# Kernel optimization log

Measured on AMD Instinct MI355X. Metric: run time of the kernel, lower is better.

Reference implementation:

```python
import jax, jax.numpy as jnp
from jax import lax
import numpy as np

LAM = 0.95          # config.agent.return_lambda
HORIZON = 333.0     # config.agent.horizon
# slowtar=True, contdisc=False

B, T, D, H = 1024, 16, 5120, 1024


def _mlp(feat, w1, b1, w2, b2, w3, b3):
    # critic MLP -> scalar mean per (b, t); [B,T,D] -> [B,T]
    h = jax.nn.silu(jnp.einsum('btd,dh->bth', feat, w1) + b1)
    h = jax.nn.silu(jnp.einsum('bth,hk->btk', h, w2) + b2)
    return jnp.einsum('bth,h->bt', h, w3) + b3[0]


def setup_inputs() -> dict:
    key = jax.random.key(0)
    ks = jax.random.split(key, 10)
    sc1 = 1.0 / np.sqrt(D)
    sc2 = 1.0 / np.sqrt(H)
    return {
        'feat': jax.random.normal(ks[0], (B, T, D), jnp.float32),
        'rew': jax.random.normal(ks[1], (B, T), jnp.float32),
        'cont': jax.random.uniform(ks[2], (B, T), jnp.float32),
        'net_w1': jax.random.normal(ks[3], (D, H), jnp.float32) * sc1,
        'net_b1': jnp.zeros((H,), jnp.float32),
        'net_w2': jax.random.normal(ks[4], (H, H), jnp.float32) * sc2,
        'net_b2': jnp.zeros((H,), jnp.float32),
        'net_w3': jax.random.normal(ks[5], (H,), jnp.float32) * sc2,
        'net_b3': jnp.zeros((1,), jnp.float32),
        'slow_w1': jax.random.normal(ks[6], (D, H), jnp.float32) * sc1,
        'slow_b1': jnp.zeros((H,), jnp.float32),
        'slow_w2': jax.random.normal(ks[7], (H, H), jnp.float32) * sc2,
        'slow_b2': jnp.zeros((H,), jnp.float32),
        'slow_w3': jax.random.normal(ks[8], (H,), jnp.float32) * sc2,
        'slow_b3': jnp.zeros((1,), jnp.float32),
        'voffset': jax.random.normal(ks[9], (1,), jnp.float32),
        'vscale': jax.random.uniform(jax.random.fold_in(key, 99), (1,), jnp.float32, minval=0.5, maxval=1.5),
    }


def reference(feat, rew, cont, net_w1, net_b1, net_w2, net_b2, net_w3, net_b3,
              slow_w1, slow_b1, slow_w2, slow_b2, slow_w3, slow_b3, voffset, vscale):
    critic = _mlp(feat, net_w1, net_b1, net_w2, net_b2, net_w3, net_b3)        # [B,T]
    slowcritic = _mlp(feat, slow_w1, slow_b1, slow_w2, slow_b2, slow_w3, slow_b3)
    val = critic * vscale[0] + voffset[0]
    slowval = slowcritic * vscale[0] + voffset[0]
    tarval = slowval  # slowtar = True
    discount = 1.0 - 1.0 / HORIZON  # contdisc = False
    disc = cont[:, 1:] * discount                                 # [B,T-1]
    interm = rew[:, 1:] + (1.0 - LAM) * disc * tarval[:, 1:]      # [B,T-1]

    def step(carry, xs):
        i_t, d_t = xs
        r = i_t + d_t * LAM * carry
        return r, r

    # reversed linear recurrence over time: rets[t] = interm[t] + disc[t]*lam*rets[t+1]
    _, ys = lax.scan(step, tarval[:, -1], (interm.T, disc.T), reverse=True)  # [T-1,B]
    ret = ys.T                                                    # [B,T-1]
    return rew, ret, tarval, critic, slowcritic
```

## Files before the change

### kernel.cpp

```cpp
#include <hip/hip_runtime.h>
#include <stdint.h>

typedef unsigned short u16;
typedef __attribute__((ext_vector_type(8))) __bf16 bf16x8;
typedef __attribute__((ext_vector_type(8))) u16 u16x8;
typedef __attribute__((ext_vector_type(4))) u16 u16x4;
typedef __attribute__((ext_vector_type(4))) float f32x4;

#define LAM 0.95f
#define DISCOUNT (1.0f - 1.0f / 333.0f)

constexpr int Bsz = 1024, Tsz = 16, Dsz = 5120, Hsz = 1024;
constexpr int Msz = Bsz * Tsz;
constexpr int Nsz = 2 * Hsz;
constexpr int ES = 136;

__device__ __forceinline__ u16 f2bf(float x) {
  union { float f; uint32_t u; } un; un.f = x;
  uint32_t u = un.u;
  return (u16)((u + 0x7FFFu + ((u >> 16) & 1u)) >> 16);
}
__device__ __forceinline__ void async16(const void* g, void* l) {
  __builtin_amdgcn_global_load_lds(
      (const __attribute__((address_space(1))) uint32_t*)g,
      (__attribute__((address_space(3))) uint32_t*)l, 16, 0, 0);
}

__global__ __launch_bounds__(256) void transpose_cvt(
    const float* __restrict__ src, u16* __restrict__ dst, int K, int N) {
  __shared__ float tile[64][65];
  int k0 = blockIdx.x * 64, n0 = blockIdx.y * 64;
  int tid = threadIdx.x;
#pragma unroll
  for (int i = 0; i < 4; ++i) {
    int idx = i * 256 + tid, rr = idx >> 4, c4 = (idx & 15) * 4;
    float4 v = *(const float4*)&src[(size_t)(k0 + rr) * N + n0 + c4];
    tile[rr][c4 + 0] = v.x; tile[rr][c4 + 1] = v.y;
    tile[rr][c4 + 2] = v.z; tile[rr][c4 + 3] = v.w;
  }
  __syncthreads();
#pragma unroll
  for (int i = 0; i < 4; ++i) {
    int idx = i * 256 + tid, rr = idx >> 4, c4 = (idx & 15) * 4;
    u16x4 o;
    o[0] = f2bf(tile[c4 + 0][rr]); o[1] = f2bf(tile[c4 + 1][rr]);
    o[2] = f2bf(tile[c4 + 2][rr]); o[3] = f2bf(tile[c4 + 3][rr]);
    *(u16x4*)&dst[(size_t)(n0 + rr) * K + k0 + c4] = o;
  }
}

__global__ void prep_small(const float* nb1, const float* sb1, const float* nb2,
                           const float* sb2, const float* nw3, const float* sw3,
                           float* bias1, float* bias2, float* w3cat,
                           float* accN, float* accS) {
  int i = blockIdx.x * 256 + threadIdx.x;
  if (i < 1024) { bias1[i] = nb1[i]; bias2[i] = nb2[i]; w3cat[i] = nw3[i]; }
  else if (i < 2048) { bias1[i] = sb1[i - 1024]; bias2[i] = sb2[i - 1024]; w3cat[i] = sw3[i - 1024]; }
  for (int j = i; j < Msz; j += gridDim.x * 256) { accN[j] = 0.f; accS[j] = 0.f; }
}

__global__ void cvt_f32_to_bf16(const float* __restrict__ src, u16* __restrict__ dst, int n4) {
  int i = blockIdx.x * 256 + threadIdx.x;
  int stride = gridDim.x * 256;
  for (; i < n4; i += stride) {
    float4 v = ((const float4*)src)[i];
    u16x4 o; o[0] = f2bf(v.x); o[1] = f2bf(v.y); o[2] = f2bf(v.z); o[3] = f2bf(v.w);
    ((u16x4*)dst)[i] = o;
  }
}

template <int MODE, bool A_F32>
__global__ __launch_bounds__(256) void gemm_fused(
    const void* __restrict__ Ap, const u16* __restrict__ Bp,
    const float* __restrict__ bias, u16* __restrict__ Out,
    const float* __restrict__ w3cat, float* __restrict__ accN, float* __restrict__ accS,
    int K, int lda, int a_half_off) {
  __shared__ __align__(16) u16 smem[(MODE == 0) ? (128 * ES) : 16384];
  u16* ldsA = smem;
  u16* ldsB = smem + 8192;

  const int tid = threadIdx.x;
  const int lane = tid & 63;
  const int wv = tid >> 6;
  const int wm = (wv >> 1) << 6;
  const int wn = (wv & 1) << 6;
  const int lm = lane & 15, lq = lane >> 4, l7 = lane & 7;

  const int blk = blockIdx.x;
  const int xcd = blk & 7;
  const int l = blk >> 3;
  const int quad = l >> 6;
  const int mi = l & 7, ni = (l >> 3) & 7;
  const int mt = xcd * 16 + ((quad & 1) << 3) + mi;
  const int nt = ((quad >> 1) << 3) + ni;
  const int m0 = mt << 7, n0 = nt << 7;
  const int a_off = (n0 >= Hsz) ? a_half_off : 0;

  const u16* bsrc[4];
  const float* asrcf[4];
  const u16* asrcb[4];
  u16* ldsAd[4];
  u16* ldsBd[4];
#pragma unroll
  for (int i = 0; i < 4; ++i) {
    int cid = i * 256 + tid;
    int row = cid >> 3, ch = cid & 7;
    int kp = ch ^ (row & 7);
    bsrc[i] = Bp + (size_t)(n0 + row) * K + kp * 8;
    if (A_F32) asrcf[i] = (const float*)Ap + (size_t)(m0 + row) * lda + a_off + kp * 8;
    else       asrcb[i] = (const u16*)Ap + (size_t)(m0 + row) * lda + a_off + kp * 8;
    ldsAd[i] = &ldsA[cid * 8];
    ldsBd[i] = &ldsB[cid * 8];
  }

  int rA[4], rB[4];
#pragma unroll
  for (int t = 0; t < 4; ++t) {
    rA[t] = (wm + t * 16 + lm) * 64;
    rB[t] = (wn + t * 16 + lm) * 64;
  }

  f32x4 acc[4][4];
#pragma unroll
  for (int a = 0; a < 4; ++a)
#pragma unroll
    for (int b = 0; b < 4; ++b) acc[a][b] = f32x4{0.f, 0.f, 0.f, 0.f};

  for (int kt = 0; kt < K; kt += 64) {
#pragma unroll
    for (int i = 0; i < 4; ++i) async16(bsrc[i] + kt, ldsBd[i]);
    if (A_F32) {
      float4 v0[4], v1[4];
#pragma unroll
      for (int i = 0; i < 4; ++i) {
        const float* p = asrcf[i] + kt;
        v0[i] = *(const float4*)p;
        v1[i] = *(const float4*)(p + 4);
      }
#pragma unroll
      for (int i = 0; i < 4; ++i) {
        u16x8 pk;
        pk[0] = f2bf(v0[i].x); pk[1] = f2bf(v0[i].y); pk[2] = f2bf(v0[i].z); pk[3] = f2bf(v0[i].w);
        pk[4] = f2bf(v1[i].x); pk[5] = f2bf(v1[i].y); pk[6] = f2bf(v1[i].z); pk[7] = f2bf(v1[i].w);
        *(u16x8*)ldsAd[i] = pk;
      }
    } else {
#pragma unroll
      for (int i = 0; i < 4; ++i) async16(asrcb[i] + kt, ldsAd[i]);
    }
    __syncthreads();
#pragma unroll
    for (int ks = 0; ks < 2; ++ks) {
      const int ck = ((ks << 2) + lq) ^ l7;
      bf16x8 af[4], bfr[4];
#pragma unroll
      for (int t = 0; t < 4; ++t) af[t] = *(const bf16x8*)&ldsA[rA[t] + ck * 8];
#pragma unroll
      for (int t = 0; t < 4; ++t) bfr[t] = *(const bf16x8*)&ldsB[rB[t] + ck * 8];
#pragma unroll
      for (int a = 0; a < 4; ++a)
#pragma unroll
        for (int b = 0; b < 4; ++b)
          acc[a][b] = __builtin_amdgcn_mfma_f32_16x16x32_bf16(bfr[b], af[a], acc[a][b], 0, 0, 0);
    }
    __syncthreads();
  }

  if (MODE == 0) {
#pragma unroll
    for (int a = 0; a < 4; ++a) {
      int ml = wm + a * 16 + lm;
#pragma unroll
      for (int b = 0; b < 4; ++b) {
        int nb = wn + b * 16 + lq * 4;
        u16x4 pk;
#pragma unroll
        for (int rr = 0; rr < 4; ++rr) {
          float v = acc[a][b][rr] + bias[n0 + nb + rr];
          v = v * (1.0f / (1.0f + __expf(-v)));
          pk[rr] = f2bf(v);
        }
        *(u16x4*)&smem[ml * ES + nb] = pk;
      }
    }
    __syncthreads();
#pragma unroll
    for (int i = 0; i < 8; ++i) {
      int r = i * 16 + (tid >> 4);
      int c = (tid & 15) * 8;
      u16x8 vv = *(const u16x8*)&smem[r * ES + c];
      *(u16x8*)&Out[(size_t)(m0 + r) * Nsz + n0 + c] = vv;
    }
  } else {
    float pr[4] = {0.f, 0.f, 0.f, 0.f};
#pragma unroll
    for (int a = 0; a < 4; ++a) {
#pragma unroll
      for (int b = 0; b < 4; ++b) {
        int nb = n0 + wn + b * 16 + lq * 4;
#pragma unroll
        for (int rr = 0; rr < 4; ++rr) {
          float v = acc[a][b][rr] + bias[nb + rr];
          v = v * (1.0f / (1.0f + __expf(-v)));
          pr[a] += v * w3cat[nb + rr];
        }
      }
    }
    float* accp = (n0 < Hsz) ? accN : accS;
#pragma unroll
    for (int a = 0; a < 4; ++a) {
      pr[a] += __shfl_xor(pr[a], 16);
      pr[a] += __shfl_xor(pr[a], 32);
      if (lq == 0) atomicAdd(&accp[m0 + wm + a * 16 + lm], pr[a]);
    }
  }
}

__global__ void finalize_scan(const float* __restrict__ accN, const float* __restrict__ accS,
                              const float* __restrict__ nb3, const float* __restrict__ sb3,
                              const float* __restrict__ voff, const float* __restrict__ vscl,
                              const float* __restrict__ rew, const float* __restrict__ cont,
                              float* __restrict__ o_rew, float* __restrict__ o_ret,
                              float* __restrict__ o_tar, float* __restrict__ o_cri,
                              float* __restrict__ o_slo) {
  __shared__ float star[Tsz], srew[Tsz], scont[Tsz];
  int b = blockIdx.x;
  int t = threadIdx.x;
  if (t < Tsz) {
    int m = b * Tsz + t;
    float c = accN[m] + nb3[0];
    float s = accS[m] + sb3[0];
    float tv = s * vscl[0] + voff[0];
    o_cri[m] = c; o_slo[m] = s; o_tar[m] = tv;
    float rw = rew[m];
    o_rew[m] = rw;
    star[t] = tv; srew[t] = rw; scont[t] = cont[m];
  }
  __syncthreads();
  if (t == 0) {
    float carry = star[Tsz - 1];
    for (int k = Tsz - 2; k >= 0; --k) {
      float d = scont[k + 1] * DISCOUNT;
      carry = srew[k + 1] + (1.0f - LAM) * d * star[k + 1] + d * LAM * carry;
      o_ret[b * (Tsz - 1) + k] = carry;
    }
  }
}

constexpr size_t WT1_OFF = 0;
constexpr size_t WT1_BYTES = (size_t)Nsz * Dsz * 2;
constexpr size_t WT2_OFF = WT1_OFF + WT1_BYTES;
constexpr size_t WT2_BYTES = (size_t)Nsz * Hsz * 2;
constexpr size_t B1_OFF = WT2_OFF + WT2_BYTES;
constexpr size_t B2_OFF = B1_OFF + 8192;
constexpr size_t W3_OFF = B2_OFF + 8192;
constexpr size_t ACCN_OFF = W3_OFF + 8192;
constexpr size_t ACCS_OFF = ACCN_OFF + (size_t)Msz * 4;
constexpr size_t H1_OFF = ACCS_OFF + (size_t)Msz * 4;
constexpr size_t H_BYTES = (size_t)Msz * Nsz * 2;
constexpr size_t FEATB_OFF = H1_OFF + H_BYTES;
constexpr size_t FEATB_BYTES = (size_t)Msz * Dsz * 2;
constexpr size_t NEED_BIG = FEATB_OFF + FEATB_BYTES;

extern "C" void kernel_launch(void* const* d_in, const int* in_sizes, int n_in,
                              void* d_out, int out_size, void* d_ws, size_t ws_size,
                              hipStream_t stream) {
  const float* feat = (const float*)d_in[0];
  const float* rew  = (const float*)d_in[1];
  const float* cont = (const float*)d_in[2];
  const float* nw1  = (const float*)d_in[3];
  const float* nb1  = (const float*)d_in[4];
  const float* nw2  = (const float*)d_in[5];
  const float* nb2  = (const float*)d_in[6];
  const float* nw3  = (const float*)d_in[7];
  const float* nb3  = (const float*)d_in[8];
  const float* sw1  = (const float*)d_in[9];
  const float* sb1  = (const float*)d_in[10];
  const float* sw2  = (const float*)d_in[11];
  const float* sb2  = (const float*)d_in[12];
  const float* sw3  = (const float*)d_in[13];
  const float* sb3  = (const float*)d_in[14];
  const float* voff = (const float*)d_in[15];
  const float* vscl = (const float*)d_in[16];

  char* ws = (char*)d_ws;
  u16* wt1 = (u16*)(ws + WT1_OFF);
  u16* wt2 = (u16*)(ws + WT2_OFF);
  float* bias1 = (float*)(ws + B1_OFF);
  float* bias2 = (float*)(ws + B2_OFF);
  float* w3cat = (float*)(ws + W3_OFF);
  float* accN = (float*)(ws + ACCN_OFF);
  float* accS = (float*)(ws + ACCS_OFF);
  u16* h1 = (u16*)(ws + H1_OFF);
  u16* featb = (u16*)(ws + FEATB_OFF);
  const bool big = ws_size >= NEED_BIG;

  float* out = (float*)d_out;
  float* o_rew = out;
  float* o_ret = out + 16384;
  float* o_tar = out + 31744;
  float* o_cri = out + 48128;
  float* o_slo = out + 64512;

  transpose_cvt<<<dim3(Dsz / 64, Hsz / 64), 256, 0, stream>>>(nw1, wt1, Dsz, Hsz);
  transpose_cvt<<<dim3(Dsz / 64, Hsz / 64), 256, 0, stream>>>(sw1, wt1 + (size_t)Hsz * Dsz, Dsz, Hsz);
  transpose_cvt<<<dim3(Hsz / 64, Hsz / 64), 256, 0, stream>>>(nw2, wt2, Hsz, Hsz);
  transpose_cvt<<<dim3(Hsz / 64, Hsz / 64), 256, 0, stream>>>(sw2, wt2 + (size_t)Hsz * Hsz, Hsz, Hsz);
  prep_small<<<8, 256, 0, stream>>>(nb1, sb1, nb2, sb2, nw3, sw3, bias1, bias2, w3cat, accN, accS);

  const int gemm_grid = (Msz / 128) * (Nsz / 128);
  if (big) {
    cvt_f32_to_bf16<<<4096, 256, 0, stream>>>(feat, featb, Msz * Dsz / 4);
    gemm_fused<0, false><<<gemm_grid, 256, 0, stream>>>(
        featb, wt1, bias1, h1, nullptr, nullptr, nullptr, Dsz, Dsz, 0);
  } else {
    gemm_fused<0, true><<<gemm_grid, 256, 0, stream>>>(
        feat, wt1, bias1, h1, nullptr, nullptr, nullptr, Dsz, Dsz, 0);
  }
  gemm_fused<1, false><<<gemm_grid, 256, 0, stream>>>(
      h1, wt2, bias2, nullptr, w3cat, accN, accS, Hsz, Nsz, Hsz);
  finalize_scan<<<Bsz, 64, 0, stream>>>(accN, accS, nb3, sb3, voff, vscl, rew, cont,
                                        o_rew, o_ret, o_tar, o_cri, o_slo);
}
```

Before: 1.043 ms.

## Add dedicated 256x128-tile GEMM1 kernel with XCD-aware block mapping

New measurement: 1.268 ms. +21.5%, slower.

```diff
diff --git a/kernel.cpp b/kernel.cpp
--- a/kernel.cpp
+++ b/kernel.cpp
@@ -66,6 +66,119 @@
     float4 v = ((const float4*)src)[i];
     u16x4 o; o[0] = f2bf(v.x); o[1] = f2bf(v.y); o[2] = f2bf(v.z); o[3] = f2bf(v.w);
     ((u16x4*)dst)[i] = o;
+  }
+}
+
+__global__ __launch_bounds__(256) void gemm1_k(
+    const u16* __restrict__ Ap, const u16* __restrict__ Bp,
+    const float* __restrict__ bias, u16* __restrict__ Out, int K) {
+  __shared__ __align__(16) u16 smem[24576];
+  u16* ldsA = smem;
+  u16* ldsB = smem + 16384;
+
+  const int tid = threadIdx.x;
+  const int lane = tid & 63;
+  const int wv = tid >> 6;
+  const int wm = (wv >> 1) * 128;
+  const int wn = (wv & 1) * 64;
+  const int lm = lane & 15, lq = lane >> 4, l7 = lane & 7;
+
+  const int blk = blockIdx.x;
+  const int xcd = blk & 7;
+  const int l = blk >> 3;
+  const int half_ = l >> 6;
+  const int mi = l & 7, ni = (l >> 3) & 7;
+  const int m0 = (xcd * 8 + mi) << 8;
+  const int n0 = ((half_ << 3) + ni) << 7;
+
+  const u16* asrc[8]; u16* ldsAd[8];
+  const u16* bsrc[4]; u16* ldsBd[4];
+#pragma unroll
+  for (int i = 0; i < 8; ++i) {
+    int cid = i * 256 + tid;
+    int row = cid >> 3, ch = cid & 7;
+    int kp = ch ^ (row & 7);
+    asrc[i] = Ap + (size_t)(m0 + row) * K + kp * 8;
+    ldsAd[i] = &ldsA[cid * 8];
+  }
+#pragma unroll
+  for (int i = 0; i < 4; ++i) {
+    int cid = i * 256 + tid;
+    int row = cid >> 3, ch = cid & 7;
+    int kp = ch ^ (row & 7);
+    bsrc[i] = Bp + (size_t)(n0 + row) * K + kp * 8;
+    ldsBd[i] = &ldsB[cid * 8];
+  }
+
+  int rA[8], rB[4];
+#pragma unroll
+  for (int t = 0; t < 8; ++t) rA[t] = (wm + t * 16 + lm) * 64;
+#pragma unroll
+  for (int t = 0; t < 4; ++t) rB[t] = (wn + t * 16 + lm) * 64;
+
+  f32x4 acc[8][4];
+#pragma unroll
+  for (int a = 0; a < 8; ++a)
+#pragma unroll
+    for (int b = 0; b < 4; ++b) acc[a][b] = f32x4{0.f, 0.f, 0.f, 0.f};
+
+  for (int kt = 0; kt < K; kt += 64) {
+#pragma unroll
+    for (int i = 0; i < 4; ++i) async16(bsrc[i] + kt, ldsBd[i]);
+#pragma unroll
+    for (int i = 0; i < 8; ++i) async16(asrc[i] + kt, ldsAd[i]);
+    __syncthreads();
+#pragma unroll
+    for (int ks = 0; ks < 2; ++ks) {
+      const int ck = ((ks << 2) + lq) ^ l7;
+      bf16x8 bfr[4];
+#pragma unroll
+      for (int t = 0; t < 4; ++t) bfr[t] = *(const bf16x8*)&ldsB[rB[t] + ck * 8];
+#pragma unroll
+      for (int h = 0; h < 2; ++h) {
+        bf16x8 af[4];
+#pragma unroll
+        for (int t = 0; t < 4; ++t) af[t] = *(const bf16x8*)&ldsA[rA[h * 4 + t] + ck * 8];
+#pragma unroll
+        for (int a = 0; a < 4; ++a)
+#pragma unroll
+          for (int b = 0; b < 4; ++b)
+            acc[h * 4 + a][b] =
+                __builtin_amdgcn_mfma_f32_16x16x32_bf16(bfr[b], af[a], acc[h * 4 + a][b], 0, 0, 0);
+      }
+    }
+    __syncthreads();
+  }
+
+#pragma unroll
+  for (int p = 0; p < 2; ++p) {
+    if ((wv >> 1) == p) {
+#pragma unroll
+      for (int a = 0; a < 8; ++a) {
+        int ml = a * 16 + lm;
+#pragma unroll
+        for (int b = 0; b < 4; ++b) {
+          int nb = wn + b * 16 + lq * 4;
+          u16x4 pk;
+#pragma unroll
+          for (int rr = 0; rr < 4; ++rr) {
+            float v = acc[a][b][rr] + bias[n0 + nb + rr];
+            v = v * (1.0f / (1.0f + __expf(-v)));
+            pk[rr] = f2bf(v);
+          }
+          *(u16x4*)&smem[ml * ES + nb] = pk;
+        }
+      }
+    }
+    __syncthreads();
+#pragma unroll
+    for (int i = 0; i < 8; ++i) {
+      int r = i * 16 + (tid >> 4);
+      int c = (tid & 15) * 8;
+      u16x8 vv = *(const u16x8*)&smem[r * ES + c];
+      *(u16x8*)&Out[(size_t)(m0 + p * 128 + r) * Nsz + n0 + c] = vv;
+    }
+    __syncthreads();
   }
 }
 
@@ -308,16 +421,14 @@
   transpose_cvt<<<dim3(Hsz / 64, Hsz / 64), 256, 0, stream>>>(sw2, wt2 + (size_t)Hsz * Hsz, Hsz, Hsz);
   prep_small<<<8, 256, 0, stream>>>(nb1, sb1, nb2, sb2, nw3, sw3, bias1, bias2, w3cat, accN, accS);
 
-  const int gemm_grid = (Msz / 128) * (Nsz / 128);
   if (big) {
     cvt_f32_to_bf16<<<4096, 256, 0, stream>>>(feat, featb, Msz * Dsz / 4);
-    gemm_fused<0, false><<<gemm_grid, 256, 0, stream>>>(
-        featb, wt1, bias1, h1, nullptr, nullptr, nullptr, Dsz, Dsz, 0);
+    gemm1_k<<<(Msz / 256) * (Nsz / 128), 256, 0, stream>>>(featb, wt1, bias1, h1, Dsz);
   } else {
-    gemm_fused<0, true><<<gemm_grid, 256, 0, stream>>>(
+    gemm_fused<0, true><<<(Msz / 128) * (Nsz / 128), 256, 0, stream>>>(
         feat, wt1, bias1, h1, nullptr, nullptr, nullptr, Dsz, Dsz, 0);
   }
-  gemm_fused<1, false><<<gemm_grid, 256, 0, stream>>>(
+  gemm_fused<1, false><<<(Msz / 128) * (Nsz / 128), 256, 0, stream>>>(
       h1, wt2, bias2, nullptr, w3cat, accN, accS, Hsz, Nsz, Hsz);
   finalize_scan<<<Bsz, 64, 0, stream>>>(accN, accS, nb3, sb3, voff, vscl, rew, cont,
                                         o_rew, o_ret, o_tar, o_cri, o_slo);
```
